# Kernel optimization log

Hardware: AMD Instinct MI355X
Metric: run time of the kernel (lower is better)

Reference implementation:

```python
import jax, jax.numpy as jnp
import numpy as np

N_NODES = 50000
N_EDGES = 800000
D = 96
H2 = 32
OUT = 4


def _glorot(key, shape):
    fan_in, fan_out = shape[0], shape[1]
    lim = (6.0 / (fan_in + fan_out)) ** 0.5
    return jax.random.uniform(key, shape, jnp.float32, -lim, lim)


def setup_inputs() -> dict:
    key = jax.random.key(0)
    ks = jax.random.split(key, 12)
    x = jax.random.normal(ks[0], (N_NODES, D), jnp.float32)
    edge_index = jax.random.randint(ks[1], (2, N_EDGES), 0, N_NODES, jnp.int32)
    return {
        "x": x,
        "edge_index": edge_index,
        "eps1": jnp.float32(0.0),
        "eps2": jnp.float32(0.0),
        "W1a": _glorot(ks[2], (D, D)),  "b1a": jnp.zeros((D,), jnp.float32),
        "W1b": _glorot(ks[3], (D, D)),  "b1b": jnp.zeros((D,), jnp.float32),
        "W2a": _glorot(ks[4], (D, H2)), "b2a": jnp.zeros((H2,), jnp.float32),
        "W2b": _glorot(ks[5], (H2, H2)),"b2b": jnp.zeros((H2,), jnp.float32),
        "Wh": _glorot(ks[6], (H2, OUT)),"bh": jnp.zeros((OUT,), jnp.float32),
    }


def _gin_agg(h, src, dst):
    # sum_{j in N(i)} h_j : gather source features, scatter-add to destination
    return jax.ops.segment_sum(h[src], dst, num_segments=N_NODES)


def reference(x, edge_index, eps1, eps2, W1a, b1a, W1b, b1b, W2a, b2a, W2b, b2b, Wh, bh):
    src, dst = edge_index[0], edge_index[1]

    # GIN layer 1: mlp1((1+eps1)*x + agg(x)), then outer ReLU (dropout is eval-mode identity)
    z = (1.0 + eps1) * x + _gin_agg(x, src, dst)           # [N, D]
    h = jax.nn.relu(z @ W1a + b1a) @ W1b + b1b             # mlp1
    h = jax.nn.relu(h)

    # GIN layer 2: mlp2((1+eps2)*h + agg(h)), then outer ReLU
    z2 = (1.0 + eps2) * h + _gin_agg(h, src, dst)          # [N, D]
    h2 = jax.nn.relu(z2 @ W2a + b2a) @ W2b + b2b           # mlp2 -> [N, 32]
    h2 = jax.nn.relu(h2)

    return h2 @ Wh + bh                                    # [N, 4]
```

## Files before the change

kernel.cpp:

```cpp
#include <hip/hip_runtime.h>

#define NN 50000
#define NE 800000
#define DD 96
#define HH 32
#define OO 4
#define ELLW 64
#define NBUCK 196
#define BCAP 8192

typedef unsigned short ushort_t;
typedef unsigned int uint_t;
typedef __attribute__((ext_vector_type(8))) short short8;
typedef __attribute__((ext_vector_type(4))) float f32x4;

__device__ inline ushort_t f2bf(float f) {
    uint_t b = __float_as_uint(f);
    return (ushort_t)((b + 0x7fffu + ((b >> 16) & 1u)) >> 16);
}

__device__ inline void addbf8(float* a, uint4 u) {
    a[0] += __uint_as_float(u.x << 16);
    a[1] += __uint_as_float(u.x & 0xffff0000u);
    a[2] += __uint_as_float(u.y << 16);
    a[3] += __uint_as_float(u.y & 0xffff0000u);
    a[4] += __uint_as_float(u.z << 16);
    a[5] += __uint_as_float(u.z & 0xffff0000u);
    a[6] += __uint_as_float(u.w << 16);
    a[7] += __uint_as_float(u.w & 0xffff0000u);
}


#define BA_B   196
#define WF_B   7
#define MT1    (NN / 16)
#define MFMA1_B ((MT1 + 3) / 4)

__global__ void k1(const int* __restrict__ edges, int* __restrict__ bcnt,
                   uint_t* __restrict__ packed,
                   const float* __restrict__ W1b, const float* __restrict__ W2a,
                   const float* __restrict__ W2b, const float* __restrict__ Wh,
                   ushort_t* __restrict__ wf,
                   const float* __restrict__ x, const float* __restrict__ W1a,
                   ushort_t* __restrict__ y1) {
    __shared__ __align__(16) ushort_t lds[1152 * 8];
    int b = blockIdx.x;
    int thr = threadIdx.x;

    if (b < BA_B) {
        int* hist = (int*)lds;
        int* basesh = hist + NBUCK;
        if (thr < NBUCK) hist[thr] = 0;
        __syncthreads();
#pragma unroll
        for (int k = 0; k < 4; ++k) {
            int t4 = b * 1024 + k * 256 + thr;
            if (t4 < NE / 4) {
                int4 tt = ((const int4*)(edges + NE))[t4];
                atomicAdd(&hist[tt.x >> 8], 1);
                atomicAdd(&hist[tt.y >> 8], 1);
                atomicAdd(&hist[tt.z >> 8], 1);
                atomicAdd(&hist[tt.w >> 8], 1);
            }
        }
        __syncthreads();
        if (thr < NBUCK) {
            int c = hist[thr];
            basesh[thr] = c ? atomicAdd(&bcnt[thr], c) : 0;
        }
        __syncthreads();
        if (thr < NBUCK) hist[thr] = 0;
        __syncthreads();
#pragma unroll
        for (int k = 0; k < 4; ++k) {
            int t4 = b * 1024 + k * 256 + thr;
            if (t4 < NE / 4) {
                int4 ss = ((const int4*)edges)[t4];
                int4 tt = ((const int4*)(edges + NE))[t4];
                int b0 = tt.x >> 8, b1 = tt.y >> 8, b2 = tt.z >> 8, b3 = tt.w >> 8;
                int p0 = basesh[b0] + atomicAdd(&hist[b0], 1);
                int p1 = basesh[b1] + atomicAdd(&hist[b1], 1);
                int p2 = basesh[b2] + atomicAdd(&hist[b2], 1);
                int p3 = basesh[b3] + atomicAdd(&hist[b3], 1);
                if (p0 < BCAP) packed[(size_t)b0 * BCAP + p0] = ((uint_t)ss.x << 8) | (tt.x & 255);
                if (p1 < BCAP) packed[(size_t)b1 * BCAP + p1] = ((uint_t)ss.y << 8) | (tt.y & 255);
                if (p2 < BCAP) packed[(size_t)b2 * BCAP + p2] = ((uint_t)ss.z << 8) | (tt.z & 255);
                if (p3 < BCAP) packed[(size_t)b3 * BCAP + p3] = ((uint_t)ss.w << 8) | (tt.w & 255);
            }
        }
        return;
    }
    b -= BA_B;

    if (b < WF_B) {
        int tw = b * 256 + thr;
        if (tw < 1728) {
            ushort_t v[8];
            ushort_t* dst;
            if (tw < 1152) {
                int fl = tw;
                int lane = fl & 63, fc = fl >> 6;
                int c = fc % 3, nt = fc / 3;
                int kb = c * 32 + (lane >> 4) * 8;
                int col = nt * 16 + (lane & 15);
#pragma unroll
                for (int j = 0; j < 8; ++j) v[j] = f2bf(W1b[(size_t)(kb + j) * DD + col]);
                dst = wf + (size_t)fl * 8;
            } else if (tw < 1536) {
                int fl = tw - 1152;
                int lane = fl & 63, fc = fl >> 6;
                int c = fc % 3, nt = fc / 3;
                int kb = c * 32 + (lane >> 4) * 8;
                int col = nt * 16 + (lane & 15);
#pragma unroll
                for (int j = 0; j < 8; ++j) v[j] = f2bf(W2a[(size_t)(kb + j) * HH + col]);
                dst = wf + 9216 + (size_t)fl * 8;
            } else if (tw < 1664) {
                int fl = tw - 1536;
                int lane = fl & 63, nt = fl >> 6;
                int kb = (lane >> 4) * 8;
                int col = nt * 16 + (lane & 15);
#pragma unroll
                for (int j = 0; j < 8; ++j) v[j] = f2bf(W2b[(size_t)(kb + j) * HH + col]);
                dst = wf + 12288 + (size_t)fl * 8;
            } else {
                int fl = tw - 1664;
                int lane = fl;
                int kb = (lane >> 4) * 8;
                int col = lane & 15;
#pragma unroll
                for (int j = 0; j < 8; ++j)
                    v[j] = (col < OO) ? f2bf(Wh[(size_t)(kb + j) * OO + col]) : (ushort_t)0;
                dst = wf + 13312 + (size_t)fl * 8;
            }
            *(uint4*)dst = *(uint4*)v;
        }
        return;
    }
    b -= WF_B;

    constexpr int KC = 3, NT = 6;
    for (int fl = thr; fl < 1152; fl += 256) {
        int lane_f = fl & 63;
        int fc = fl >> 6;
        int c = fc % 3, nt = fc / 3;
        int kb = c * 32 + (lane_f >> 4) * 8;
        int col = nt * 16 + (lane_f & 15);
        ushort_t v[8];
#pragma unroll
        for (int j = 0; j < 8; ++j)
            v[j] = f2bf(W1a[(size_t)(kb + j) * DD + col]);
        *(uint4*)(lds + (size_t)fl * 8) = *(uint4*)v;
    }
    __syncthreads();

    int lane = thr & 63;
    int widx = thr >> 6;
    int tile = b * 4 + widx;
    if (tile >= MT1) return;
    int row0 = tile * 16;
    int q = lane >> 4;
    int l16 = lane & 15;

    short8 bf[NT][KC];
#pragma unroll
    for (int nt = 0; nt < NT; ++nt)
#pragma unroll
        for (int c = 0; c < KC; ++c)
            bf[nt][c] = *(short8*)(lds + ((size_t)(nt * 3 + c) * 64 + lane) * 8);

    short8 af[KC];
#pragma unroll
    for (int c = 0; c < KC; ++c) {
        const float* ap = x + (size_t)(row0 + l16) * DD + c * 32 + q * 8;
        float4 f0 = *(const float4*)ap;
        float4 f1 = *(const float4*)(ap + 4);
        ushort_t v[8] = {f2bf(f0.x), f2bf(f0.y), f2bf(f0.z), f2bf(f0.w),
                         f2bf(f1.x), f2bf(f1.y), f2bf(f1.z), f2bf(f1.w)};
        af[c] = *(short8*)v;
    }

    f32x4 acc[NT];
#pragma unroll
    for (int nt = 0; nt < NT; ++nt) acc[nt] = (f32x4){0.f, 0.f, 0.f, 0.f};
#pragma unroll
    for (int nt = 0; nt < NT; ++nt)
#pragma unroll
        for (int c = 0; c < KC; ++c)
            acc[nt] = __builtin_amdgcn_mfma_f32_16x16x32_bf16(af[c], bf[nt][c], acc[nt], 0, 0, 0);

#pragma unroll
    for (int nt = 0; nt < NT; ++nt) {
        int s = nt >> 1;
        int c32 = (nt & 1) * 16 + l16;
#pragma unroll
        for (int r = 0; r < 4; ++r)
            y1[(size_t)s * NN * 32 + (size_t)(row0 + q * 4 + r) * 32 + c32] = f2bf(acc[nt][r]);
    }
}


__global__ void k2(const int* __restrict__ bcnt, const uint_t* __restrict__ packed,
                   ushort_t* __restrict__ ell, int* __restrict__ deg) {
    __shared__ int curL[256];
    int b = blockIdx.x;
    int thr = threadIdx.x;
    int n0 = b * 256;
    curL[thr] = 0;
    __syncthreads();
    int cnt = min(bcnt[b], BCAP);
    const uint_t* pk = packed + (size_t)b * BCAP;
    for (int e = thr; e < cnt; e += 256) {
        uint_t u = pk[e];
        int doff = u & 255;
        int src = u >> 8;
        int p = atomicAdd(&curL[doff], 1);
        if (p < ELLW) ell[(size_t)(n0 + doff) * ELLW + p] = (ushort_t)src;
    }
    __syncthreads();
    if (n0 + thr < NN) deg[n0 + thr] = curL[thr];
}


#define HSTRIDE 104

__global__ void k_aggmm(const ushort_t* __restrict__ y1, const int* __restrict__ deg,
                        const ushort_t* __restrict__ ell, const float* __restrict__ eps_p,
                        const float* __restrict__ b1a, const ushort_t* __restrict__ wf,
                        const float* __restrict__ b1b, ushort_t* __restrict__ y2) {
    constexpr int KC = 3, NT1 = 6, NT2 = 2;
    __shared__ __align__(16) ushort_t hT[64 * HSTRIDE];
    __shared__ __align__(16) ushort_t erL[64 * ELLW];
    __shared__ int degL[64];
    int thr = threadIdx.x;
    int i0 = blockIdx.x * 64;

    for (int t = thr; t < 64 * 8; t += 256) {
        int r = t >> 3, c8 = t & 7;
        int ii = i0 + r;
        uint4 val;
        if (ii < NN) val = ((const uint4*)(ell + (size_t)ii * ELLW))[c8];
        else { val.x = 0; val.y = 0; val.z = 0; val.w = 0; }
        *(uint4*)&erL[r * 64 + c8 * 8] = val;
    }
    if (thr < 64) degL[thr] = (i0 + thr < NN) ? min(deg[i0 + thr], ELLW) : 0;
    __syncthreads();

    int g = thr >> 2;
    int u = thr & 3;
    int i = i0 + g;

    if (i < NN) {
        const ushort_t* er = &erL[g * 64];
        int d = degL[g];
        float e = 1.0f + eps_p[0];
        const float4* b4 = (const float4*)b1a;
        ushort_t* dstg = &hT[g * HSTRIDE + u * 8];
#pragma unroll 1
        for (int s = 0; s < 3; ++s) {
            const uint4* ysS = (const uint4*)(y1 + (size_t)s * NN * 32);
            float a0[8] = {0,0,0,0,0,0,0,0}, a1[8] = {0,0,0,0,0,0,0,0};
            float a2[8] = {0,0,0,0,0,0,0,0}, a3[8] = {0,0,0,0,0,0,0,0};
            int p = 0;
            for (; p + 3 < d; p += 4) {
                int s0 = er[p], s1 = er[p + 1], s2 = er[p + 2], s3 = er[p + 3];
                uint4 f0 = ysS[(size_t)s0 * 4 + u];
                uint4 f1 = ysS[(size_t)s1 * 4 + u];
                uint4 f2 = ysS[(size_t)s2 * 4 + u];
                uint4 f3 = ysS[(size_t)s3 * 4 + u];
                addbf8(a0, f0); addbf8(a1, f1); addbf8(a2, f2); addbf8(a3, f3);
            }
            for (; p < d; ++p) addbf8(a0, ysS[(size_t)er[p] * 4 + u]);

            uint4 su = ysS[(size_t)i * 4 + u];
            float s8[8];
            s8[0] = __uint_as_float(su.x << 16); s8[1] = __uint_as_float(su.x & 0xffff0000u);
            s8[2] = __uint_as_float(su.y << 16); s8[3] = __uint_as_float(su.y & 0xffff0000u);
            s8[4] = __uint_as_float(su.z << 16); s8[5] = __uint_as_float(su.z & 0xffff0000u);
            s8[6] = __uint_as_float(su.w << 16); s8[7] = __uint_as_float(su.w & 0xffff0000u);
            float4 bl = b4[s * 8 + u * 2];
            float4 bh2 = b4[s * 8 + u * 2 + 1];
            float bb[8] = {bl.x, bl.y, bl.z, bl.w, bh2.x, bh2.y, bh2.z, bh2.w};
            ushort_t r[8];
#pragma unroll
            for (int k = 0; k < 8; ++k) {
                float vv = fmaf(e, s8[k], (a0[k] + a1[k]) + (a2[k] + a3[k])) + bb[k];
                r[k] = f2bf(fmaxf(vv, 0.0f));
            }
            *(uint4*)(dstg + s * 32) = *(uint4*)r;
        }
    }
    __syncthreads();

    int lane = thr & 63;
    int widx = thr >> 6;
    int tile = blockIdx.x * 4 + widx;
    if (tile >= MT1) return;
    int row0 = tile * 16;
    int q = lane >> 4;
    int l16 = lane & 15;
    const short8* bfp1 = (const short8*)wf;
    const short8* bfp2 = (const short8*)(wf + 9216);

    short8 bf[NT1][KC];
#pragma unroll
    for (int nt = 0; nt < NT1; ++nt)
#pragma unroll
        for (int c = 0; c < KC; ++c)
            bf[nt][c] = bfp1[(nt * KC + c) * 64 + lane];

    short8 af2[KC];
#pragma unroll
    for (int c = 0; c < KC; ++c) {
        uint4 av = *(const uint4*)&hT[(widx * 16 + l16) * HSTRIDE + c * 32 + q * 8];
        af2[c] = *(short8*)&av;
    }

    f32x4 acc[NT1];
#pragma unroll
    for (int nt = 0; nt < NT1; ++nt) acc[nt] = (f32x4){0.f, 0.f, 0.f, 0.f};
#pragma unroll
    for (int nt = 0; nt < NT1; ++nt)
#pragma unroll
        for (int c = 0; c < KC; ++c)
            acc[nt] = __builtin_amdgcn_mfma_f32_16x16x32_bf16(af2[c], bf[nt][c], acc[nt], 0, 0, 0);

    __syncthreads();
#pragma unroll
    for (int nt = 0; nt < NT1; ++nt) {
        int col = nt * 16 + l16;
        float bv = b1b[col];
#pragma unroll
        for (int r = 0; r < 4; ++r)
            hT[(widx * 16 + q * 4 + r) * HSTRIDE + col] = f2bf(fmaxf(acc[nt][r] + bv, 0.0f));
    }
    __syncthreads();

    short8 af3[KC];
#pragma unroll
    for (int c = 0; c < KC; ++c) {
        uint4 av = *(const uint4*)&hT[(widx * 16 + l16) * HSTRIDE + c * 32 + q * 8];
        af3[c] = *(short8*)&av;
    }
    short8 bf2[NT2][KC];
#pragma unroll
    for (int nt = 0; nt < NT2; ++nt)
#pragma unroll
        for (int c = 0; c < KC; ++c)
            bf2[nt][c] = bfp2[(nt * KC + c) * 64 + lane];

    f32x4 acc2[NT2];
#pragma unroll
    for (int nt = 0; nt < NT2; ++nt) acc2[nt] = (f32x4){0.f, 0.f, 0.f, 0.f};
#pragma unroll
    for (int nt = 0; nt < NT2; ++nt)
#pragma unroll
        for (int c = 0; c < KC; ++c)
            acc2[nt] = __builtin_amdgcn_mfma_f32_16x16x32_bf16(af3[c], bf2[nt][c], acc2[nt], 0, 0, 0);

#pragma unroll
    for (int nt = 0; nt < NT2; ++nt) {
        int col = nt * 16 + l16;
#pragma unroll
        for (int r = 0; r < 4; ++r)
            y2[(size_t)(row0 + q * 4 + r) * HH + col] = f2bf(acc2[nt][r]);
    }
}


#define TS2 40

__global__ void k_agg2tail(const ushort_t* __restrict__ y2, const int* __restrict__ deg,
                           const ushort_t* __restrict__ ell, const float* __restrict__ eps_p,
                           const float* __restrict__ b2a, const float* __restrict__ b2b,
                           const float* __restrict__ bhp, const ushort_t* __restrict__ wf,
                           float* __restrict__ out) {
    __shared__ __align__(16) ushort_t erL[64 * ELLW];
    __shared__ int degL[64];
    __shared__ __align__(16) ushort_t t2T[64 * TS2];
    __shared__ __align__(16) ushort_t hB[4][16 * TS2];
    int thr = threadIdx.x;
    int i0 = blockIdx.x * 64;

    for (int t = thr; t < 64 * 8; t += 256) {
        int r = t >> 3, c8 = t & 7;
        int ii = i0 + r;
        uint4 val;
        if (ii < NN) val = ((const uint4*)(ell + (size_t)ii * ELLW))[c8];
        else { val.x = 0; val.y = 0; val.z = 0; val.w = 0; }
        *(uint4*)&erL[r * 64 + c8 * 8] = val;
    }
    if (thr < 64) degL[thr] = (i0 + thr < NN) ? min(deg[i0 + thr], ELLW) : 0;
    __syncthreads();

    int g = thr >> 2;
    int u = thr & 3;
    int i = i0 + g;

    if (i < NN) {
        const ushort_t* er = &erL[g * 64];
        int d = degL[g];
        const uint4* y4 = (const uint4*)y2;
        float a0[8] = {0,0,0,0,0,0,0,0}, a1[8] = {0,0,0,0,0,0,0,0};
        float a2[8] = {0,0,0,0,0,0,0,0}, a3[8] = {0,0,0,0,0,0,0,0};
        int p = 0;
        for (; p + 3 < d; p += 4) {
            int s0 = er[p], s1 = er[p + 1], s2 = er[p + 2], s3 = er[p + 3];
            uint4 f0 = y4[(size_t)s0 * 4 + u];
            uint4 f1 = y4[(size_t)s1 * 4 + u];
            uint4 f2 = y4[(size_t)s2 * 4 + u];
            uint4 f3 = y4[(size_t)s3 * 4 + u];
            addbf8(a0, f0); addbf8(a1, f1); addbf8(a2, f2); addbf8(a3, f3);
        }
        for (; p < d; ++p) addbf8(a0, y4[(size_t)er[p] * 4 + u]);

        uint4 su = y4[(size_t)i * 4 + u];
        float s8[8];
        s8[0] = __uint_as_float(su.x << 16); s8[1] = __uint_as_float(su.x & 0xffff0000u);
        s8[2] = __uint_as_float(su.y << 16); s8[3] = __uint_as_float(su.y & 0xffff0000u);
        s8[4] = __uint_as_float(su.z << 16); s8[5] = __uint_as_float(su.z & 0xffff0000u);
        s8[6] = __uint_as_float(su.w << 16); s8[7] = __uint_as_float(su.w & 0xffff0000u);
        float4 bl = ((const float4*)b2a)[u * 2];
        float4 bh2 = ((const float4*)b2a)[u * 2 + 1];
        float bb[8] = {bl.x, bl.y, bl.z, bl.w, bh2.x, bh2.y, bh2.z, bh2.w};
        float e = 1.0f + eps_p[0];
        ushort_t r[8];
#pragma unroll
        for (int k = 0; k < 8; ++k) {
            float vv = fmaf(e, s8[k], (a0[k] + a1[k]) + (a2[k] + a3[k])) + bb[k];
            r[k] = f2bf(fmaxf(vv, 0.0f));
        }
        *(uint4*)&t2T[g * TS2 + u * 8] = *(uint4*)r;
    }
    __syncthreads();

    int lane = thr & 63;
    int widx = thr >> 6;
    int tile = blockIdx.x * 4 + widx;
    if (tile >= MT1) return;
    int row0 = tile * 16;
    int q = lane >> 4;
    int l16 = lane & 15;

    uint4 av = *(const uint4*)&t2T[(widx * 16 + l16) * TS2 + q * 8];
    short8 afA = *(short8*)&av;
    const short8* bfW2b = (const short8*)(wf + 12288);
    const short8* bfWh  = (const short8*)(wf + 13312);

    f32x4 acc2[2];
#pragma unroll
    for (int nt = 0; nt < 2; ++nt) {
        acc2[nt] = (f32x4){0.f, 0.f, 0.f, 0.f};
        acc2[nt] = __builtin_amdgcn_mfma_f32_16x16x32_bf16(afA, bfW2b[nt * 64 + lane],
                                                           acc2[nt], 0, 0, 0);
    }

#pragma unroll
    for (int nt = 0; nt < 2; ++nt) {
        int col = nt * 16 + l16;
        float bv = b2b[col];
#pragma unroll
        for (int r = 0; r < 4; ++r)
            hB[widx][(q * 4 + r) * TS2 + col] = f2bf(fmaxf(acc2[nt][r] + bv, 0.0f));
    }

    uint4 av2 = *(const uint4*)&hB[widx][l16 * TS2 + q * 8];
    short8 afH = *(short8*)&av2;
    f32x4 acch = (f32x4){0.f, 0.f, 0.f, 0.f};
    acch = __builtin_amdgcn_mfma_f32_16x16x32_bf16(afH, bfWh[lane], acch, 0, 0, 0);

    if (l16 < OO) {
        float bv = bhp[l16];
#pragma unroll
        for (int r = 0; r < 4; ++r)
            out[(size_t)(row0 + q * 4 + r) * OO + l16] = acch[r] + bv;
    }
}


extern "C" void kernel_launch(void* const* d_in, const int* in_sizes, int n_in,
                              void* d_out, int out_size, void* d_ws, size_t ws_size,
                              hipStream_t stream) {
    const float* x    = (const float*)d_in[0];
    const int*   edges= (const int*)d_in[1];
    const float* eps1 = (const float*)d_in[2];
    const float* eps2 = (const float*)d_in[3];
    const float* W1a  = (const float*)d_in[4];
    const float* b1a  = (const float*)d_in[5];
    const float* W1b  = (const float*)d_in[6];
    const float* b1b  = (const float*)d_in[7];
    const float* W2a  = (const float*)d_in[8];
    const float* b2a  = (const float*)d_in[9];
    const float* W2b  = (const float*)d_in[10];
    const float* b2b  = (const float*)d_in[11];
    const float* Wh   = (const float*)d_in[12];
    const float* bh   = (const float*)d_in[13];

    auto al = [](size_t n) { return (n + 255) / 256 * 256; };
    char* w = (char*)d_ws;
    int*      bcnt   = (int*)w;      w += al((size_t)NBUCK * 4);
    uint_t*   packed = (uint_t*)w;   w += al((size_t)NBUCK * BCAP * 4);
    int*      deg    = (int*)w;      w += al((size_t)NN * 4);
    ushort_t* ell    = (ushort_t*)w; w += al((size_t)NN * ELLW * 2);
    ushort_t* wf     = (ushort_t*)w; w += al((size_t)13824 * 2);
    ushort_t* y1     = (ushort_t*)w; w += al((size_t)NN * DD * 2);
    ushort_t* y2     = (ushort_t*)w; w += al((size_t)NN * HH * 2);

    hipMemsetAsync(bcnt, 0, (size_t)NBUCK * 4, stream);
    k1<<<BA_B + WF_B + MFMA1_B, 256, 0, stream>>>(edges, bcnt, packed, W1b, W2a, W2b, Wh,
                                                  wf, x, W1a, y1);
    k2<<<NBUCK, 256, 0, stream>>>(bcnt, packed, ell, deg);
    k_aggmm<<<MFMA1_B, 256, 0, stream>>>(y1, deg, ell, eps1, b1a, wf, b1b, y2);
    k_agg2tail<<<(NN + 63) / 64, 256, 0, stream>>>(y2, deg, ell, eps2, b2a, b2b, bh, wf,
                                                   (float*)d_out);
}
```

Measured before the change: 153.0 us.

## Fuse ELL construction into aggregation kernels, dropping the separate ELL build pass

Removes the k2 kernel that wrote a global ELL adjacency and degree array. Each aggregation block now rebuilds its own 64-row ELL slice in LDS by scanning its 256-node bucket of packed edges, filtering to its rows, and inserting with LDS atomics. This saves a kernel launch and the global ELL write and reread. In exchange, each bucket is scanned redundantly by four blocks in each of two kernels, and neighbor order within a row is now nondeterministic.

```diff
diff --git a/kernel.cpp b/kernel.cpp
--- a/kernel.cpp
+++ b/kernel.cpp
@@ -28,6 +28,27 @@
     a[5] += __uint_as_float(u.z & 0xffff0000u);
     a[6] += __uint_as_float(u.w << 16);
     a[7] += __uint_as_float(u.w & 0xffff0000u);
+}
+
+__device__ inline void build_ell_lds(const int* __restrict__ bcnt,
+                                     const uint_t* __restrict__ packed,
+                                     int i0, int thr,
+                                     ushort_t* erL, int* cntL) {
+    if (thr < 64) cntL[thr] = 0;
+    __syncthreads();
+    int bk = i0 >> 8;
+    int w0 = i0 & 255;
+    int cnt = min(bcnt[bk], BCAP);
+    const uint_t* pk = packed + (size_t)bk * BCAP;
+    for (int e = thr; e < cnt; e += 256) {
+        uint_t u = pk[e];
+        int doff = (int)(u & 255u) - w0;
+        if ((unsigned)doff < 64u) {
+            int p = atomicAdd(&cntL[doff], 1);
+            if (p < ELLW) erL[doff * 64 + p] = (ushort_t)(u >> 8);
+        }
+    }
+    __syncthreads();
 }
 
 
@@ -200,51 +221,20 @@
 }
 
 
-__global__ void k2(const int* __restrict__ bcnt, const uint_t* __restrict__ packed,
-                   ushort_t* __restrict__ ell, int* __restrict__ deg) {
-    __shared__ int curL[256];
-    int b = blockIdx.x;
-    int thr = threadIdx.x;
-    int n0 = b * 256;
-    curL[thr] = 0;
-    __syncthreads();
-    int cnt = min(bcnt[b], BCAP);
-    const uint_t* pk = packed + (size_t)b * BCAP;
-    for (int e = thr; e < cnt; e += 256) {
-        uint_t u = pk[e];
-        int doff = u & 255;
-        int src = u >> 8;
-        int p = atomicAdd(&curL[doff], 1);
-        if (p < ELLW) ell[(size_t)(n0 + doff) * ELLW + p] = (ushort_t)src;
-    }
-    __syncthreads();
-    if (n0 + thr < NN) deg[n0 + thr] = curL[thr];
-}
-
-
 #define HSTRIDE 104
 
-__global__ void k_aggmm(const ushort_t* __restrict__ y1, const int* __restrict__ deg,
-                        const ushort_t* __restrict__ ell, const float* __restrict__ eps_p,
+__global__ void k_aggmm(const int* __restrict__ bcnt, const uint_t* __restrict__ packed,
+                        const ushort_t* __restrict__ y1, const float* __restrict__ eps_p,
                         const float* __restrict__ b1a, const ushort_t* __restrict__ wf,
                         const float* __restrict__ b1b, ushort_t* __restrict__ y2) {
     constexpr int KC = 3, NT1 = 6, NT2 = 2;
     __shared__ __align__(16) ushort_t hT[64 * HSTRIDE];
     __shared__ __align__(16) ushort_t erL[64 * ELLW];
-    __shared__ int degL[64];
+    __shared__ int cntL[64];
     int thr = threadIdx.x;
     int i0 = blockIdx.x * 64;
 
-    for (int t = thr; t < 64 * 8; t += 256) {
-        int r = t >> 3, c8 = t & 7;
-        int ii = i0 + r;
-        uint4 val;
-        if (ii < NN) val = ((const uint4*)(ell + (size_t)ii * ELLW))[c8];
-        else { val.x = 0; val.y = 0; val.z = 0; val.w = 0; }
-        *(uint4*)&erL[r * 64 + c8 * 8] = val;
-    }
-    if (thr < 64) degL[thr] = (i0 + thr < NN) ? min(deg[i0 + thr], ELLW) : 0;
-    __syncthreads();
+    build_ell_lds(bcnt, packed, i0, thr, erL, cntL);
 
     int g = thr >> 2;
     int u = thr & 3;
@@ -252,7 +242,7 @@
 
     if (i < NN) {
         const ushort_t* er = &erL[g * 64];
-        int d = degL[g];
+        int d = min(cntL[g], ELLW);
         float e = 1.0f + eps_p[0];
         const float4* b4 = (const float4*)b1a;
         ushort_t* dstg = &hT[g * HSTRIDE + u * 8];
@@ -370,28 +360,19 @@
 
 #define TS2 40
 
-__global__ void k_agg2tail(const ushort_t* __restrict__ y2, const int* __restrict__ deg,
-                           const ushort_t* __restrict__ ell, const float* __restrict__ eps_p,
+__global__ void k_agg2tail(const int* __restrict__ bcnt, const uint_t* __restrict__ packed,
+                           const ushort_t* __restrict__ y2, const float* __restrict__ eps_p,
                            const float* __restrict__ b2a, const float* __restrict__ b2b,
                            const float* __restrict__ bhp, const ushort_t* __restrict__ wf,
                            float* __restrict__ out) {
     __shared__ __align__(16) ushort_t erL[64 * ELLW];
-    __shared__ int degL[64];
+    __shared__ int cntL[64];
     __shared__ __align__(16) ushort_t t2T[64 * TS2];
     __shared__ __align__(16) ushort_t hB[4][16 * TS2];
     int thr = threadIdx.x;
     int i0 = blockIdx.x * 64;
 
-    for (int t = thr; t < 64 * 8; t += 256) {
-        int r = t >> 3, c8 = t & 7;
-        int ii = i0 + r;
-        uint4 val;
-        if (ii < NN) val = ((const uint4*)(ell + (size_t)ii * ELLW))[c8];
-        else { val.x = 0; val.y = 0; val.z = 0; val.w = 0; }
-        *(uint4*)&erL[r * 64 + c8 * 8] = val;
-    }
-    if (thr < 64) degL[thr] = (i0 + thr < NN) ? min(deg[i0 + thr], ELLW) : 0;
-    __syncthreads();
+    build_ell_lds(bcnt, packed, i0, thr, erL, cntL);
 
     int g = thr >> 2;
     int u = thr & 3;
@@ -399,7 +380,7 @@
 
     if (i < NN) {
         const ushort_t* er = &erL[g * 64];
-        int d = degL[g];
+        int d = min(cntL[g], ELLW);
         const uint4* y4 = (const uint4*)y2;
         float a0[8] = {0,0,0,0,0,0,0,0}, a1[8] = {0,0,0,0,0,0,0,0};
         float a2[8] = {0,0,0,0,0,0,0,0}, a3[8] = {0,0,0,0,0,0,0,0};
@@ -500,8 +481,6 @@
     char* w = (char*)d_ws;
     int*      bcnt   = (int*)w;      w += al((size_t)NBUCK * 4);
     uint_t*   packed = (uint_t*)w;   w += al((size_t)NBUCK * BCAP * 4);
-    int*      deg    = (int*)w;      w += al((size_t)NN * 4);
-    ushort_t* ell    = (ushort_t*)w; w += al((size_t)NN * ELLW * 2);
     ushort_t* wf     = (ushort_t*)w; w += al((size_t)13824 * 2);
     ushort_t* y1     = (ushort_t*)w; w += al((size_t)NN * DD * 2);
     ushort_t* y2     = (ushort_t*)w; w += al((size_t)NN * HH * 2);
@@ -509,8 +488,7 @@
     hipMemsetAsync(bcnt, 0, (size_t)NBUCK * 4, stream);
     k1<<<BA_B + WF_B + MFMA1_B, 256, 0, stream>>>(edges, bcnt, packed, W1b, W2a, W2b, Wh,
                                                   wf, x, W1a, y1);
-    k2<<<NBUCK, 256, 0, stream>>>(bcnt, packed, ell, deg);
-    k_aggmm<<<MFMA1_B, 256, 0, stream>>>(y1, deg, ell, eps1, b1a, wf, b1b, y2);
-    k_agg2tail<<<(NN + 63) / 64, 256, 0, stream>>>(y2, deg, ell, eps2, b2a, b2b, bh, wf,
-                                                   (float*)d_out);
-}
+    k_aggmm<<<MFMA1_B, 256, 0, stream>>>(bcnt, packed, y1, eps1, b1a, wf, b1b, y2);
+    k_agg2tail<<<MFMA1_B, 256, 0, stream>>>(bcnt, packed, y2, eps2, b2a, b2b, bh, wf,
+                                            (float*)d_out);
+}
```

Measured after the change: 152.6 us, median of 2. No clear change (-0.3%).
